# Kernel tuning notes

Hardware: AMD Instinct MI355X
Metric: run time of the kernel (lower is better)

Reference implementation:

```python
import jax, jax.numpy as jnp
import numpy as np

VOCAB = 62
HID = 100
NLAYERS = 3
B, T = 512, 1024


def setup_inputs() -> dict:
    key = jax.random.key(0)
    ks = jax.random.split(key, 8)
    s = 1.0 / np.sqrt(HID)  # PyTorch RNN init scale
    input_ids = jax.random.randint(ks[0], (B, T), 0, VOCAB, dtype=jnp.int32)
    emb = jax.random.normal(ks[1], (VOCAB, HID), dtype=jnp.float32)
    W_ih = jax.random.uniform(ks[2], (NLAYERS, HID, HID), jnp.float32, -s, s)
    W_hh = jax.random.uniform(ks[3], (NLAYERS, HID, HID), jnp.float32, -s, s)
    b_ih = jax.random.uniform(ks[4], (NLAYERS, HID), jnp.float32, -s, s)
    b_hh = jax.random.uniform(ks[5], (NLAYERS, HID), jnp.float32, -s, s)
    W_dec = jax.random.uniform(ks[6], (VOCAB, HID), jnp.float32, -s, s)
    b_dec = jax.random.uniform(ks[7], (VOCAB,), jnp.float32, -s, s)
    return {
        "input_ids": input_ids,
        "emb": emb,
        "W_ih": W_ih,
        "W_hh": W_hh,
        "b_ih": b_ih,
        "b_hh": b_hh,
        "W_dec": W_dec,
        "b_dec": b_dec,
    }


def _rnn_forward(x, W_ih, W_hh, b_ih, b_hh):
    # x: [B, T, H]; multi-layer tanh RNN, zero initial hidden (hidden=None path)
    bsz = x.shape[0]
    finals = []
    layer_in = jnp.swapaxes(x, 0, 1)  # time-major [T, B, H]
    for l in range(NLAYERS):
        Wi, Wh = W_ih[l], W_hh[l]
        bi, bh = b_ih[l], b_hh[l]
        # precompute input projection for whole sequence (one big GEMM)
        xin = jnp.einsum("tbh,kh->tbk", layer_in, Wi) + bi + bh

        def step(h, xt):
            h_new = jnp.tanh(xt + h @ Wh.T)
            return h_new, h_new

        h0 = jnp.zeros((bsz, HID), dtype=x.dtype)
        h_final, ys = jax.lax.scan(step, h0, xin)
        finals.append(h_final)
        layer_in = ys
    out = jnp.swapaxes(layer_in, 0, 1)  # [B, T, H]
    hidden = jnp.stack(finals, axis=0)  # [NLAYERS, B, H]
    return out, hidden


def reference(input_ids, emb, W_ih, W_hh, b_ih, b_hh, W_dec, b_dec):
    x = emb[input_ids]  # [B, T, H] embedding lookup
    rnn_out, hidden = _rnn_forward(x, W_ih, W_hh, b_ih, b_hh)
    logits = jnp.einsum("bth,vh->btv", rnn_out, W_dec) + b_dec  # [B, T, VOCAB]
    return logits, hidden
```

## Files before the change

### kernel.cpp

```cpp
#include <hip/hip_runtime.h>

#define BB 512
#define TT 1024
#define HH 100
#define VV 62
#define BTV (512*1024*62)

#define OFF_EP  52428800
#define OFF_WU  52435200
#define OFF_BS  52491200
#define OFF_WDT 52491400
#define OFF_BDP 52497800

typedef float v2f __attribute__((ext_vector_type(2)));

__device__ inline float tanh_fast(float x){
  float ax = fabsf(x);
  float e  = __expf(2.0f*ax);
  float r  = 1.0f - __fdividef(2.0f, e + 1.0f);
  return copysignf(r, x);
}

__device__ inline float dpp_xor1(float x){
  return __int_as_float(__builtin_amdgcn_update_dpp(0, __float_as_int(x), 0xB1, 0xF, 0xF, true));
}
__device__ inline float dpp_xor2(float x){
  return __int_as_float(__builtin_amdgcn_update_dpp(0, __float_as_int(x), 0x4E, 0xF, 0xF, true));
}

__global__ void prep_kernel(
    const float* __restrict__ emb, const float* __restrict__ W_ih,
    const float* __restrict__ W_hh,
    const float* __restrict__ b_ih, const float* __restrict__ b_hh,
    const float* __restrict__ W_dec, const float* __restrict__ b_dec,
    float* __restrict__ ws)
{
  int g = blockIdx.x*256 + threadIdx.x;
  if (g < 6200){
    int v = g/100, k = g%100;
    float a = b_ih[k] + b_hh[k];
    const float* er = emb + v*100;
    const float* wr = W_ih + k*100;
    for (int h=0; h<100; h++) a = fmaf(er[h], wr[h], a);
    ws[OFF_EP + v*100 + k] = a;
  } else if (g < 62200){
    int i = g - 6200;
    int u, base;
    if (i < 11200){ u=0; base=i; }
    else if (i < 33600){ u=1; base=i-11200; }
    else { u=2; base=i-33600; }
    int lane = base/112, e = base%112;
    int j = e/56, c = e%56;
    float val;
    if (u==0){
      int q = lane&1, rp = lane>>1;
      int r = rp + 50*j;
      int col = 56*q + c;
      val = (col < HH) ? W_hh[r*HH + col] : 0.f;
    } else {
      int q = lane&3, rp = lane>>2;
      int r = rp + 50*j;
      if (q < 2){
        int col = 56*q + c;
        val = (col < HH) ? W_ih[u*10000 + r*HH + col] : 0.f;
      } else {
        int col = 56*(q-2) + c;
        val = (col < HH) ? W_hh[u*10000 + r*HH + col] : 0.f;
      }
    }
    ws[OFF_WU + i] = val;
  } else if (g < 62400){
    int i = g - 62200;
    int l = i/100 + 1, k = i%100;
    ws[OFF_BS + i] = b_ih[l*100+k] + b_hh[l*100+k];
  } else if (g < 68800){
    int i = g - 62400;
    int h = i/64, v = i%64;
    ws[OFF_WDT + i] = (v < VV) ? W_dec[v*100 + h] : 0.f;
  } else if (g < 68864){
    int i = g - 68800;
    ws[OFF_BDP + i] = (i < VV) ? b_dec[i] : 0.f;
  }
}

__global__ __launch_bounds__(512, 2) void fused_rnn(
    const int* __restrict__ ids, const float* __restrict__ ws,
    float* __restrict__ buf, float* __restrict__ hid)
{
  __shared__ float ep_s[6200];
  __shared__ int   ids_s[2][TT];
  __shared__ float hs[2][2][3][112];

  const int tid = threadIdx.x;
  const int bA = blockIdx.x, bB = blockIdx.x + 256;

  int u, l; bool act = true;
  if (tid < 100){ u=0; l=tid; }
  else if (tid < 300){ u=1; l=tid-100; }
  else if (tid < 500){ u=2; l=tid-300; }
  else { u=2; l=199; act=false; }

  int q, rp, lv, col0;
  if (u==0){ q = l&1; rp = l>>1; lv = 0; col0 = 56*q; }
  else     { q = l&3; rp = l>>2; lv = (u==1) ? ((q<2)?0:1) : ((q<2)?1:2); col0 = 56*(q&1); }

  v2f w[56];
  {
    int ubase = (u==0) ? 0 : (u==1) ? 11200 : 33600;
    const float4* ws4 = (const float4*)(ws + OFF_WU + ubase + l*112);
    #pragma unroll
    for (int i=0;i<28;i++){
      float4 t = ws4[i];
      w[2*i]   = (v2f){t.x, t.y};
      w[2*i+1] = (v2f){t.z, t.w};
    }
  }
  float bias0 = 0.f, bias1 = 0.f;
  if (u != 0 && q == 0){
    const float* bs = ws + OFF_BS + (u-1)*100;
    bias0 = bs[rp]; bias1 = bs[rp+50];
  }

  for (int i=tid;i<6200;i+=512) ep_s[i] = ws[OFF_EP+i];
  for (int i=tid;i<TT;i+=512){
    ids_s[0][i] = ids[(size_t)bA*TT + i];
    ids_s[1][i] = ids[(size_t)bB*TT + i];
  }
  for (int i=tid;i<2*2*3*112;i+=512) ((float*)hs)[i] = 0.f;
  __syncthreads();

  const float4* h4 = (const float4*)hs;
  const int c4 = col0 >> 2;
  const int iA = (0*3 + lv)*28 + c4;
  const int iB = (1*3 + lv)*28 + c4;
  float* hw = (float*)hs;

  int idn = 0; float epx0 = 0.f, epx1 = 0.f;
  if (u == 0){
    int id0 = ids_s[q][0];
    epx0 = ep_s[id0*HH + rp];
    epx1 = ep_s[id0*HH + rp+50];
    idn  = ids_s[q][1];
  }
  const int X  = q >> 1;
  const int rr = rp + 50*(q & 1);
  float* stp = buf + ((size_t)(X ? bB : bA))*TT*HH + rr;

  for (int s = 0; s < TT + 2; ++s){
    const int po = (s & 1) ? 0 : 168;
    const int wo = (s & 1) ? 672 : 0;

    v2f aA0 = {bias0, 0.f}, aA1 = {bias1, 0.f};
    v2f aB0 = {bias0, 0.f}, aB1 = {bias1, 0.f};
    #pragma unroll
    for (int i=0;i<14;i++){
      float4 ha = h4[iA + po + i];
      float4 hb = h4[iB + po + i];
      v2f h0 = {ha.x, ha.y}, h1 = {ha.z, ha.w};
      v2f g0 = {hb.x, hb.y}, g1 = {hb.z, hb.w};
      aA0 = __builtin_elementwise_fma(w[2*i],    h0, aA0);
      aA0 = __builtin_elementwise_fma(w[2*i+1],  h1, aA0);
      aA1 = __builtin_elementwise_fma(w[28+2*i], h0, aA1);
      aA1 = __builtin_elementwise_fma(w[29+2*i], h1, aA1);
      aB0 = __builtin_elementwise_fma(w[2*i],    g0, aB0);
      aB0 = __builtin_elementwise_fma(w[2*i+1],  g1, aB0);
      aB1 = __builtin_elementwise_fma(w[28+2*i], g0, aB1);
      aB1 = __builtin_elementwise_fma(w[29+2*i], g1, aB1);
    }
    float zA0 = aA0.x + aA0.y;
    float zA1 = aA1.x + aA1.y;
    float zB0 = aB0.x + aB0.y;
    float zB1 = aB1.x + aB1.y;
    zA0 += dpp_xor1(zA0); zA1 += dpp_xor1(zA1);
    zB0 += dpp_xor1(zB0); zB1 += dpp_xor1(zB1);
    if (u){
      zA0 += dpp_xor2(zA0); zA1 += dpp_xor2(zA1);
      zB0 += dpp_xor2(zB0); zB1 += dpp_xor2(zB1);
    }

    if (u == 0){
      if (s < TT){
        float za = q ? zB0 : zA0;
        float zb = q ? zB1 : zA1;
        float h0v = tanh_fast(epx0 + za);
        float h1v = tanh_fast(epx1 + zb);
        hw[wo + (q*3 + 0)*112 + rp]      = h0v;
        hw[wo + (q*3 + 0)*112 + rp + 50] = h1v;
        if (s == TT-1){
          int bX = q ? bB : bA;
          hid[(size_t)bX*HH + rp]      = h0v;
          hid[(size_t)bX*HH + rp + 50] = h1v;
        }
        epx0 = ep_s[idn*HH + rp];
        epx1 = ep_s[idn*HH + rp + 50];
        idn  = ids_s[q][(s+2 < TT) ? s+2 : TT-1];
      }
    } else {
      float zs = (q & 1) ? (X ? zB1 : zA1) : (X ? zB0 : zA0);
      bool on = (u == 1) ? ((unsigned)(s-1) < TT) : (s >= 2);
      if (on & act){
        float hv = tanh_fast(zs);
        hw[wo + (X*3 + u)*112 + rr] = hv;
        if (u == 2){ *stp = hv; stp += HH; }
        int bX = X ? bB : bA;
        if (u == 1 && s == TT)     hid[((size_t)BB   + bX)*HH + rr] = hv;
        if (u == 2 && s == TT+1)   hid[((size_t)2*BB + bX)*HH + rr] = hv;
      }
    }

    asm volatile("s_waitcnt lgkmcnt(0)" ::: "memory");
    __builtin_amdgcn_s_barrier();
    asm volatile("" ::: "memory");
  }
}

__global__ __launch_bounds__(128) void dec_kernel(
    const float* __restrict__ buf, const float* __restrict__ wdt,
    const float* __restrict__ bdp, float* __restrict__ out)
{
  __shared__ float rt[100*129];
  const int tid = threadIdx.x;
  const int wg  = blockIdx.x;
  const int bb  = wg >> 3;
  const int t0  = (wg & 7) * 128;
  const float4* b4 = (const float4*)buf;
  const size_t rb = ((size_t)bb*TT + t0)*25;

  #pragma unroll
  for (int j=0;j<25;j++){
    int f = j*128 + tid;
    int i = f/25, c = f%25;
    float4 v = b4[rb + f];
    rt[(4*c+0)*129 + i] = v.x;
    rt[(4*c+1)*129 + i] = v.y;
    rt[(4*c+2)*129 + i] = v.z;
    rt[(4*c+3)*129 + i] = v.w;
  }
  __syncthreads();

  float4 acc[16];
  const float4* bd4 = (const float4*)bdp;
  #pragma unroll
  for (int j=0;j<16;j++) acc[j] = bd4[j];

  for (int h=0; h<HH; h++){
    float rv = rt[h*129 + tid];
    const float4* w4 = (const float4*)(wdt + h*64);
    #pragma unroll
    for (int j=0;j<16;j++){
      float4 w = w4[j];
      acc[j].x = fmaf(rv,w.x,acc[j].x);
      acc[j].y = fmaf(rv,w.y,acc[j].y);
      acc[j].z = fmaf(rv,w.z,acc[j].z);
      acc[j].w = fmaf(rv,w.w,acc[j].w);
    }
  }

  float2* o2 = (float2*)(out + ((size_t)bb*TT + t0 + tid)*VV);
  #pragma unroll
  for (int j=0;j<15;j++){
    o2[2*j]   = make_float2(acc[j].x, acc[j].y);
    o2[2*j+1] = make_float2(acc[j].z, acc[j].w);
  }
  o2[30] = make_float2(acc[15].x, acc[15].y);
}

extern "C" void kernel_launch(void* const* d_in, const int* in_sizes, int n_in,
                              void* d_out, int out_size, void* d_ws, size_t ws_size,
                              hipStream_t stream)
{
  const int*   ids   = (const int*)d_in[0];
  const float* emb   = (const float*)d_in[1];
  const float* W_ih  = (const float*)d_in[2];
  const float* W_hh  = (const float*)d_in[3];
  const float* b_ih  = (const float*)d_in[4];
  const float* b_hh  = (const float*)d_in[5];
  const float* W_dec = (const float*)d_in[6];
  const float* b_dec = (const float*)d_in[7];
  float* out = (float*)d_out;
  float* ws  = (float*)d_ws;
  float* buf = ws;
  float* hid = out + BTV;

  prep_kernel<<<269, 256, 0, stream>>>(emb, W_ih, W_hh, b_ih, b_hh, W_dec, b_dec, ws);
  fused_rnn <<<256, 512, 0, stream>>>(ids, ws, buf, hid);
  dec_kernel<<<4096, 128, 0, stream>>>(buf, ws+OFF_WDT, ws+OFF_BDP, out);
}
```

Baseline: 1.369 ms.

## Remap RNN weight lanes to 4-row x 28-col tiles with quad transpose-reduce

Reorganizes the per-thread weight slices of the recurrent kernel so each lane holds four output rows over a 28-column chunk instead of two rows over 56 columns. The partial sums are then combined with a DPP transpose-reduce across lane quads plus a ds_swizzle for the input/hidden halves, which shortens the serial FMA chain and LDS read per step. Padding lanes are added so groups align to quads. The decoder kernel is also switched to packed v2f FMAs. The swizzle goes through LDS hardware and adds latency, and the extra select logic could cost more than it saves on the per-step critical path.

```diff
diff --git a/kernel.cpp b/kernel.cpp
--- a/kernel.cpp
+++ b/kernel.cpp
@@ -26,6 +26,18 @@
 }
 __device__ inline float dpp_xor2(float x){
   return __int_as_float(__builtin_amdgcn_update_dpp(0, __float_as_int(x), 0x4E, 0xF, 0xF, true));
+}
+__device__ inline float swz_xor4(float x){
+  return __int_as_float(__builtin_amdgcn_ds_swizzle(__float_as_int(x), 0x101F));
+}
+
+__device__ inline float quad_txr(float a0,float a1,float a2,float a3,bool odd,bool hi){
+  float s01 = odd ? a0 : a1, k01 = odd ? a1 : a0;
+  float A  = k01 + dpp_xor1(s01);
+  float s23 = odd ? a2 : a3, k23 = odd ? a3 : a2;
+  float Bq = k23 + dpp_xor1(s23);
+  float sAB = hi ? A : Bq, kAB = hi ? Bq : A;
+  return kAB + dpp_xor2(sAB);
 }
 
 __global__ void prep_kernel(
@@ -50,23 +62,17 @@
     else if (i < 33600){ u=1; base=i-11200; }
     else { u=2; base=i-33600; }
     int lane = base/112, e = base%112;
-    int j = e/56, c = e%56;
+    int j = e/28, c = e%28;
     float val;
     if (u==0){
-      int q = lane&1, rp = lane>>1;
-      int r = rp + 50*j;
-      int col = 56*q + c;
-      val = (col < HH) ? W_hh[r*HH + col] : 0.f;
+      int gq = lane&3, rp = lane>>2;
+      int row = 4*rp + j, col = 28*gq + c;
+      val = (col < HH) ? W_hh[row*HH + col] : 0.f;
     } else {
-      int q = lane&3, rp = lane>>2;
-      int r = rp + 50*j;
-      if (q < 2){
-        int col = 56*q + c;
-        val = (col < HH) ? W_ih[u*10000 + r*HH + col] : 0.f;
-      } else {
-        int col = 56*(q-2) + c;
-        val = (col < HH) ? W_hh[u*10000 + r*HH + col] : 0.f;
-      }
+      int gq = lane&7, rp = lane>>3;
+      int row = 4*rp + j, col = 28*(gq&3) + c;
+      const float* M = (gq < 4) ? W_ih : W_hh;
+      val = (col < HH) ? M[u*10000 + row*HH + col] : 0.f;
     }
     ws[OFF_WU + i] = val;
   } else if (g < 62400){
@@ -94,32 +100,27 @@
   const int tid = threadIdx.x;
   const int bA = blockIdx.x, bB = blockIdx.x + 256;
 
-  int u, l; bool act = true;
-  if (tid < 100){ u=0; l=tid; }
-  else if (tid < 300){ u=1; l=tid-100; }
-  else if (tid < 500){ u=2; l=tid-300; }
-  else { u=2; l=199; act=false; }
-
-  int q, rp, lv, col0;
-  if (u==0){ q = l&1; rp = l>>1; lv = 0; col0 = 56*q; }
-  else     { q = l&3; rp = l>>2; lv = (u==1) ? ((q<2)?0:1) : ((q<2)?1:2); col0 = 56*(q&1); }
-
-  v2f w[56];
+  int u, l; bool act;
+  if      (tid < 100){ u=0; l=tid;     act=true;  }
+  else if (tid < 104){ u=0; l=tid-4;   act=false; }
+  else if (tid < 304){ u=1; l=tid-104; act=true;  }
+  else if (tid < 504){ u=2; l=tid-304; act=true;  }
+  else               { u=2; l=tid-312; act=false; }
+
+  int gq, rp, g3, lv;
+  if (u==0){ gq = l&3; rp = l>>2; g3 = gq; lv = 0; }
+  else     { gq = l&7; rp = l>>3; g3 = gq&3; lv = (u==1) ? (gq<4?0:1) : (gq<4?1:2); }
+  const int r = 4*rp + g3;
+  const bool odd = tid & 1, hi = tid & 2;
+
+  float4 w4[28];
   {
     int ubase = (u==0) ? 0 : (u==1) ? 11200 : 33600;
-    const float4* ws4 = (const float4*)(ws + OFF_WU + ubase + l*112);
+    const float4* wr = (const float4*)(ws + OFF_WU + ubase + l*112);
     #pragma unroll
-    for (int i=0;i<28;i++){
-      float4 t = ws4[i];
-      w[2*i]   = (v2f){t.x, t.y};
-      w[2*i+1] = (v2f){t.z, t.w};
-    }
-  }
-  float bias0 = 0.f, bias1 = 0.f;
-  if (u != 0 && q == 0){
-    const float* bs = ws + OFF_BS + (u-1)*100;
-    bias0 = bs[rp]; bias1 = bs[rp+50];
-  }
+    for (int i=0;i<28;i++) w4[i] = wr[i];
+  }
+  const float br = (u==0) ? 0.f : ws[OFF_BS + (u-1)*100 + r];
 
   for (int i=tid;i<6200;i+=512) ep_s[i] = ws[OFF_EP+i];
   for (int i=tid;i<TT;i+=512){
@@ -130,81 +131,79 @@
   __syncthreads();
 
   const float4* h4 = (const float4*)hs;
-  const int c4 = col0 >> 2;
-  const int iA = (0*3 + lv)*28 + c4;
-  const int iB = (1*3 + lv)*28 + c4;
+  const int iA = lv*28 + 7*g3;
+  const int iB = 84 + lv*28 + 7*g3;
   float* hw = (float*)hs;
 
-  int idn = 0; float epx0 = 0.f, epx1 = 0.f;
+  int idnA = 0, idnB = 0; float epxA = 0.f, epxB = 0.f;
   if (u == 0){
-    int id0 = ids_s[q][0];
-    epx0 = ep_s[id0*HH + rp];
-    epx1 = ep_s[id0*HH + rp+50];
-    idn  = ids_s[q][1];
-  }
-  const int X  = q >> 1;
-  const int rr = rp + 50*(q & 1);
-  float* stp = buf + ((size_t)(X ? bB : bA))*TT*HH + rr;
+    epxA = ep_s[ids_s[0][0]*HH + l];
+    epxB = ep_s[ids_s[1][0]*HH + l];
+    idnA = ids_s[0][1]; idnB = ids_s[1][1];
+  }
+  const int X  = gq >> 2;
+  const int bX = X ? bB : bA;
+  float* stp = buf + (size_t)bX*TT*HH + r;
 
   for (int s = 0; s < TT + 2; ++s){
     const int po = (s & 1) ? 0 : 168;
     const int wo = (s & 1) ? 672 : 0;
 
-    v2f aA0 = {bias0, 0.f}, aA1 = {bias1, 0.f};
-    v2f aB0 = {bias0, 0.f}, aB1 = {bias1, 0.f};
+    v2f aA0={0.f,0.f}, aA1={0.f,0.f}, aA2={0.f,0.f}, aA3={0.f,0.f};
+    v2f aB0={0.f,0.f}, aB1={0.f,0.f}, aB2={0.f,0.f}, aB3={0.f,0.f};
+    const float4* pA = h4 + (iA + po);
+    const float4* pB = h4 + (iB + po);
     #pragma unroll
-    for (int i=0;i<14;i++){
-      float4 ha = h4[iA + po + i];
-      float4 hb = h4[iB + po + i];
-      v2f h0 = {ha.x, ha.y}, h1 = {ha.z, ha.w};
-      v2f g0 = {hb.x, hb.y}, g1 = {hb.z, hb.w};
-      aA0 = __builtin_elementwise_fma(w[2*i],    h0, aA0);
-      aA0 = __builtin_elementwise_fma(w[2*i+1],  h1, aA0);
-      aA1 = __builtin_elementwise_fma(w[28+2*i], h0, aA1);
-      aA1 = __builtin_elementwise_fma(w[29+2*i], h1, aA1);
-      aB0 = __builtin_elementwise_fma(w[2*i],    g0, aB0);
-      aB0 = __builtin_elementwise_fma(w[2*i+1],  g1, aB0);
-      aB1 = __builtin_elementwise_fma(w[28+2*i], g0, aB1);
-      aB1 = __builtin_elementwise_fma(w[29+2*i], g1, aB1);
-    }
-    float zA0 = aA0.x + aA0.y;
-    float zA1 = aA1.x + aA1.y;
-    float zB0 = aB0.x + aB0.y;
-    float zB1 = aB1.x + aB1.y;
-    zA0 += dpp_xor1(zA0); zA1 += dpp_xor1(zA1);
-    zB0 += dpp_xor1(zB0); zB1 += dpp_xor1(zB1);
+    for (int i=0;i<7;i++){
+      float4 ha = pA[i];
+      float4 hb = pB[i];
+      v2f h0 = {ha.x,ha.y}, h1 = {ha.z,ha.w};
+      v2f g0 = {hb.x,hb.y}, g1 = {hb.z,hb.w};
+      float4 wv0 = w4[i], wv1 = w4[7+i], wv2 = w4[14+i], wv3 = w4[21+i];
+      v2f w00={wv0.x,wv0.y}, w01={wv0.z,wv0.w};
+      v2f w10={wv1.x,wv1.y}, w11={wv1.z,wv1.w};
+      v2f w20={wv2.x,wv2.y}, w21={wv2.z,wv2.w};
+      v2f w30={wv3.x,wv3.y}, w31={wv3.z,wv3.w};
+      aA0 = __builtin_elementwise_fma(w00,h0,aA0); aA0 = __builtin_elementwise_fma(w01,h1,aA0);
+      aA1 = __builtin_elementwise_fma(w10,h0,aA1); aA1 = __builtin_elementwise_fma(w11,h1,aA1);
+      aA2 = __builtin_elementwise_fma(w20,h0,aA2); aA2 = __builtin_elementwise_fma(w21,h1,aA2);
+      aA3 = __builtin_elementwise_fma(w30,h0,aA3); aA3 = __builtin_elementwise_fma(w31,h1,aA3);
+      aB0 = __builtin_elementwise_fma(w00,g0,aB0); aB0 = __builtin_elementwise_fma(w01,g1,aB0);
+      aB1 = __builtin_elementwise_fma(w10,g0,aB1); aB1 = __builtin_elementwise_fma(w11,g1,aB1);
+      aB2 = __builtin_elementwise_fma(w20,g0,aB2); aB2 = __builtin_elementwise_fma(w21,g1,aB2);
+      aB3 = __builtin_elementwise_fma(w30,g0,aB3); aB3 = __builtin_elementwise_fma(w31,g1,aB3);
+    }
+    float zA = quad_txr(aA0.x+aA0.y, aA1.x+aA1.y, aA2.x+aA2.y, aA3.x+aA3.y, odd, hi);
+    float zB = quad_txr(aB0.x+aB0.y, aB1.x+aB1.y, aB2.x+aB2.y, aB3.x+aB3.y, odd, hi);
     if (u){
-      zA0 += dpp_xor2(zA0); zA1 += dpp_xor2(zA1);
-      zB0 += dpp_xor2(zB0); zB1 += dpp_xor2(zB1);
+      zA += swz_xor4(zA);
+      zB += swz_xor4(zB);
     }
 
     if (u == 0){
-      if (s < TT){
-        float za = q ? zB0 : zA0;
-        float zb = q ? zB1 : zA1;
-        float h0v = tanh_fast(epx0 + za);
-        float h1v = tanh_fast(epx1 + zb);
-        hw[wo + (q*3 + 0)*112 + rp]      = h0v;
-        hw[wo + (q*3 + 0)*112 + rp + 50] = h1v;
+      if (act && s < TT){
+        float hA = tanh_fast(epxA + zA);
+        float hB = tanh_fast(epxB + zB);
+        hw[wo + l]       = hA;
+        hw[wo + 336 + l] = hB;
         if (s == TT-1){
-          int bX = q ? bB : bA;
-          hid[(size_t)bX*HH + rp]      = h0v;
-          hid[(size_t)bX*HH + rp + 50] = h1v;
+          hid[(size_t)bA*HH + l] = hA;
+          hid[(size_t)bB*HH + l] = hB;
         }
-        epx0 = ep_s[idn*HH + rp];
-        epx1 = ep_s[idn*HH + rp + 50];
-        idn  = ids_s[q][(s+2 < TT) ? s+2 : TT-1];
+        epxA = ep_s[idnA*HH + l];
+        epxB = ep_s[idnB*HH + l];
+        int nid = (s+2 < TT) ? s+2 : TT-1;
+        idnA = ids_s[0][nid]; idnB = ids_s[1][nid];
       }
     } else {
-      float zs = (q & 1) ? (X ? zB1 : zA1) : (X ? zB0 : zA0);
+      float z = X ? zB : zA;
       bool on = (u == 1) ? ((unsigned)(s-1) < TT) : (s >= 2);
-      if (on & act){
-        float hv = tanh_fast(zs);
-        hw[wo + (X*3 + u)*112 + rr] = hv;
+      if (act && on){
+        float hv = tanh_fast(z + br);
+        hw[wo + X*336 + u*112 + r] = hv;
         if (u == 2){ *stp = hv; stp += HH; }
-        int bX = X ? bB : bA;
-        if (u == 1 && s == TT)     hid[((size_t)BB   + bX)*HH + rr] = hv;
-        if (u == 2 && s == TT+1)   hid[((size_t)2*BB + bX)*HH + rr] = hv;
+        if (u == 1 && s == TT)     hid[((size_t)BB   + bX)*HH + r] = hv;
+        if (u == 2 && s == TT+1)   hid[((size_t)2*BB + bX)*HH + r] = hv;
       }
     }
 
@@ -238,31 +237,22 @@
   }
   __syncthreads();
 
-  float4 acc[16];
-  const float4* bd4 = (const float4*)bdp;
+  v2f acc[32];
+  const v2f* bd2 = (const v2f*)bdp;
   #pragma unroll
-  for (int j=0;j<16;j++) acc[j] = bd4[j];
+  for (int j=0;j<32;j++) acc[j] = bd2[j];
 
   for (int h=0; h<HH; h++){
     float rv = rt[h*129 + tid];
-    const float4* w4 = (const float4*)(wdt + h*64);
+    v2f rv2 = {rv, rv};
+    const v2f* w2 = (const v2f*)(wdt + h*64);
     #pragma unroll
-    for (int j=0;j<16;j++){
-      float4 w = w4[j];
-      acc[j].x = fmaf(rv,w.x,acc[j].x);
-      acc[j].y = fmaf(rv,w.y,acc[j].y);
-      acc[j].z = fmaf(rv,w.z,acc[j].z);
-      acc[j].w = fmaf(rv,w.w,acc[j].w);
-    }
+    for (int j=0;j<32;j++) acc[j] = __builtin_elementwise_fma(w2[j], rv2, acc[j]);
   }
 
   float2* o2 = (float2*)(out + ((size_t)bb*TT + t0 + tid)*VV);
   #pragma unroll
-  for (int j=0;j<15;j++){
-    o2[2*j]   = make_float2(acc[j].x, acc[j].y);
-    o2[2*j+1] = make_float2(acc[j].z, acc[j].w);
-  }
-  o2[30] = make_float2(acc[15].x, acc[15].y);
+  for (int j=0;j<31;j++) o2[j] = make_float2(acc[j].x, acc[j].y);
 }
 
 extern "C" void kernel_launch(void* const* d_in, const int* in_sizes, int n_in,
```

After: 1.421 ms. 1.04x slower.
